# Kernel tuning notes

Hardware: AMD Instinct MI355X
Metric: run time of the kernel (lower is better)

Reference implementation:

```python
import jax, jax.numpy as jnp
import numpy as np

B, C, H, W = 4, 256, 48, 48
HEADS, DH = 8, 32
INNER = HEADS * DH
HID = 128  # max(16, INNER//2)
SCALE = DH ** -0.5
EPS = 1e-6


def setup_inputs() -> dict:
    key = jax.random.key(0)
    ks = jax.random.split(key, 32)
    s = 0.02
    inp = {
        'x': jax.random.normal(ks[0], (B, C, H, W), jnp.float32),
        'rgb_input': jax.random.uniform(ks[1], (B, 3, H, W), jnp.float32),
        'wq': jax.random.normal(ks[2], (INNER, C), jnp.float32) * s,
        'bq': jnp.zeros((INNER,), jnp.float32),
        'wk': jax.random.normal(ks[3], (INNER, C), jnp.float32) * s,
        'bk': jnp.zeros((INNER,), jnp.float32),
        'wv': jax.random.normal(ks[4], (INNER, C), jnp.float32) * s,
        'bv': jnp.zeros((INNER,), jnp.float32),
        'wproj': jax.random.normal(ks[5], (C, INNER), jnp.float32) * s,
        'bproj': jnp.zeros((C,), jnp.float32),
        'c1_w': jax.random.normal(ks[6], (HID, 1, 3, 3), jnp.float32) * s,
        'c1_b': jnp.zeros((HID,), jnp.float32),
        'c2_w': jax.random.normal(ks[7], (HID, HID, 3, 3), jnp.float32) * s,
        'c2_b': jnp.zeros((HID,), jnp.float32),
        'gq_w': jax.random.normal(ks[8], (INNER, HID), jnp.float32) * s,
        'gq_b': jnp.ones((INNER,), jnp.float32),
        'bqf_w': jax.random.normal(ks[9], (INNER, HID), jnp.float32) * s,
        'bqf_b': jnp.zeros((INNER,), jnp.float32),
        'gk_w': jax.random.normal(ks[10], (INNER, HID), jnp.float32) * s,
        'gk_b': jnp.ones((INNER,), jnp.float32),
        'bkf_w': jax.random.normal(ks[11], (INNER, HID), jnp.float32) * s,
        'bkf_b': jnp.zeros((INNER,), jnp.float32),
        'gv_w': jax.random.normal(ks[12], (INNER, HID), jnp.float32) * s,
        'gv_b': jnp.ones((INNER,), jnp.float32),
        'bvf_w': jax.random.normal(ks[13], (INNER, HID), jnp.float32) * s,
        'bvf_b': jnp.zeros((INNER,), jnp.float32),
        'alpha': jnp.float32(0.1),
    }
    return inp


def _conv3(x, w, b):
    y = jax.lax.conv_general_dilated(x, w, (1, 1), 'SAME',
                                     dimension_numbers=('NCHW', 'OIHW', 'NCHW'))
    return y + b[None, :, None, None]


def _rgb_to_luma(rgb):
    y = 0.299 * rgb[:, 0:1] + 0.587 * rgb[:, 1:2] + 0.114 * rgb[:, 2:3]
    y_min = jnp.min(y, axis=(2, 3), keepdims=True)
    y_max = jnp.max(y, axis=(2, 3), keepdims=True)
    return (y - y_min) / (y_max - y_min + EPS)


def reference(x, rgb_input, wq, bq, wk, bk, wv, bv, wproj, bproj,
              c1_w, c1_b, c2_w, c2_b,
              gq_w, gq_b, bqf_w, bqf_b, gk_w, gk_b, bkf_w, bkf_b,
              gv_w, gv_b, bvf_w, bvf_b, alpha):
    Bx, Cx, Hx, Wx = x.shape
    N = Hx * Wx
    luma = _rgb_to_luma(rgb_input)  # [B,1,H,W]

    # LumaCond trunk + FiLM params (1x1 convs then global spatial mean)
    h = jax.nn.relu(_conv3(luma, c1_w, c1_b))
    h = jax.nn.relu(_conv3(h, c2_w, c2_b))
    hm = h.mean(axis=(2, 3))  # [B,HID] (mean commutes with 1x1 conv)

    def film_params(gw, gb, bw, bb):
        g = hm @ gw.T + gb  # [B, INNER]
        bta = hm @ bw.T + bb
        return (g.reshape(Bx, HEADS, DH, 1), bta.reshape(Bx, HEADS, DH, 1))

    gq, fbq = film_params(gq_w, gq_b, bqf_w, bqf_b)
    gk, fbk = film_params(gk_w, gk_b, bkf_w, bkf_b)
    gv, fbv = film_params(gv_w, gv_b, bvf_w, bvf_b)

    def proj_film(w, b, g, bta):
        t = jnp.einsum('bchw,oc->bohw', x, w) + b[None, :, None, None]
        t = t.reshape(Bx, HEADS, DH, N)
        return g * t + bta  # [B,heads,dh,N]

    q = proj_film(wq, bq, gq, fbq)
    k = proj_film(wk, bk, gk, fbk)
    v = proj_film(wv, bv, gv, fbv)

    logits = jnp.einsum('bhdn,bhdm->bhnm', q, k) * SCALE  # [B,heads,N,N]

    # luma bias: avg-pooled inverse luma, mean-centered per image
    invL = 1.0 - luma
    invL = jax.lax.reduce_window(invL, 0.0, jax.lax.add,
                                 (1, 1, 3, 3), (1, 1, 1, 1), 'SAME') / 9.0
    invL = invL.reshape(Bx, N)
    invL = invL - invL.mean(axis=-1, keepdims=True)
    logits = logits + alpha * invL[:, None, None, :]

    attn = jax.nn.softmax(logits, axis=-1)
    out = jnp.einsum('bhnm,bhdm->bhdn', attn, v)  # [B,heads,dh,N]
    out = out.reshape(Bx, INNER, Hx, Wx)
    return jnp.einsum('bchw,oc->bohw', out, wproj) + bproj[None, :, None, None]
```

## Files before the change

kernel.cpp:

```cpp
#include <hip/hip_runtime.h>


#define NSP 2304
#define WID 48

typedef __attribute__((ext_vector_type(4))) float  fvec4;
typedef __attribute__((ext_vector_type(2))) unsigned int uvec2;
typedef __attribute__((ext_vector_type(4))) unsigned int uvec4;
typedef __attribute__((ext_vector_type(8))) short  short8;
typedef __attribute__((ext_vector_type(4))) float  f32x4;

__device__ inline unsigned short f2bf(float f){
  unsigned int u = __builtin_bit_cast(unsigned int, f);
  u += 0x7fffu + ((u >> 16) & 1u);
  return (unsigned short)(u >> 16);
}
__device__ inline unsigned pack2bf(float a, float b){
#if __has_builtin(__builtin_amdgcn_cvt_pk_bf16_f32)
  typedef __attribute__((ext_vector_type(2))) __bf16 bf16x2;
  bf16x2 r = __builtin_amdgcn_cvt_pk_bf16_f32(a, b);
  return __builtin_bit_cast(unsigned, r);
#else
  return (unsigned)f2bf(a) | ((unsigned)f2bf(b) << 16);
#endif
}

__global__ __launch_bounds__(256) void k_prep(const float* __restrict__ c2w,
    const float* __restrict__ wq, const float* __restrict__ wk, const float* __restrict__ wv_,
    const float* __restrict__ wproj, const float* __restrict__ x,
    const float* __restrict__ rgb, const float* __restrict__ alphaP,
    unsigned short* __restrict__ wtb, unsigned short* __restrict__ wqkvb,
    unsigned short* __restrict__ wprojb, unsigned short* __restrict__ xt,
    float* __restrict__ luma_n, float* __restrict__ bias_a,
    float* __restrict__ hm_sum, unsigned short* __restrict__ h1p){
  __shared__ __align__(16) float sm[5120];
  int bx = blockIdx.x, t = threadIdx.x;
  if (bx < 4){
    int b = bx;
    float* ly  = sm;
    float* ll  = sm + NSP;
    float* red = sm + 2*NSP;
    float* red2= sm + 2*NSP + 256;
    {
      const uvec4 z = {0u,0u,0u,0u};
      for (int j = t; j < 196*16; j += 256){
        int cell = j >> 4, q = j & 15;
        int r, c;
        if (cell < 50)      { r = 0;           c = cell; }
        else if (cell < 100){ r = 49;          c = cell - 50; }
        else if (cell < 148){ r = cell - 99;   c = 0; }
        else                { r = cell - 147;  c = 49; }
        *(uvec4*)(h1p + ((size_t)(b*2500 + r*50 + c))*128 + q*8) = z;
      }
    }
    const float* rp = rgb + b*3*NSP;
    float lmin = 1e30f, lmax = -1e30f;
    for (int i = t; i < NSP; i += 256){
      float y = 0.299f*rp[i] + 0.587f*rp[NSP+i] + 0.114f*rp[2*NSP+i];
      ly[i] = y; lmin = fminf(lmin, y); lmax = fmaxf(lmax, y);
    }
    red[t] = lmin; red2[t] = lmax;
    __syncthreads();
    for (int s = 128; s > 0; s >>= 1){
      if (t < s){ red[t] = fminf(red[t], red[t+s]); red2[t] = fmaxf(red2[t], red2[t+s]); }
      __syncthreads();
    }
    float mn = red[0], mx = red2[0];
    float inv = 1.0f / (mx - mn + 1e-6f);
    for (int i = t; i < NSP; i += 256){
      float v = (ly[i] - mn) * inv;
      ll[i] = v;
      luma_n[b*NSP + i] = v;
    }
    if (t < 128) hm_sum[b*128 + t] = 0.f;
    __syncthreads();
    float pr[9]; float psum = 0.f;
    #pragma unroll
    for (int ii = 0; ii < 9; ++ii){
      int n = t + 256*ii;
      int row = n / WID, col = n - row*WID;
      float s2 = 0.f;
      #pragma unroll
      for (int dy = -1; dy <= 1; ++dy)
        #pragma unroll
        for (int dx = -1; dx <= 1; ++dx){
          int r2 = row+dy, c2 = col+dx;
          if (r2 >= 0 && r2 < WID && c2 >= 0 && c2 < WID) s2 += 1.0f - ll[r2*WID + c2];
        }
      pr[ii] = s2 * (1.f/9.f);
      psum += pr[ii];
    }
    __syncthreads();
    red[t] = psum;
    __syncthreads();
    for (int s = 128; s > 0; s >>= 1){
      if (t < s) red[t] += red[t+s];
      __syncthreads();
    }
    float mean = red[0] * (1.f/(float)NSP);
    float alpha = alphaP[0] * 1.4426950408889634f;
    #pragma unroll
    for (int ii = 0; ii < 9; ++ii){
      int n = t + 256*ii;
      bias_a[b*NSP + n] = alpha * (pr[ii] - mean);
    }
  } else if (bx < 1604){
    int idx = (bx - 4)*256 + t;
    if (idx < 147456){
      int ic = idx & 127, rem = idx >> 7;
      int oc = rem & 127, tap = rem >> 7;
      wtb[idx] = f2bf(c2w[(oc*128 + ic)*9 + tap]);
    } else if (idx < 344064){
      int j = idx - 147456;
      int mat = j >> 16, oc_ = j & 65535;
      const float* src = (mat == 0) ? wq : (mat == 1) ? wk : wv_;
      wqkvb[j] = f2bf(src[oc_]);
    } else {
      int j = idx - 344064;
      wprojb[j] = f2bf(wproj[j]);
    }
  } else {
    int j = bx - 1604;
    int nt = j % 36, cc = (j / 36) & 3, b = j / 144;
    unsigned short* tb = (unsigned short*)sm;
    int cl0 = t >> 4;
    int nl0 = (t & 15) * 4;
    #pragma unroll
    for (int ps_ = 0; ps_ < 4; ++ps_){
      int cl = cl0 + ps_*16;
      fvec4 v = *(const fvec4*)(x + ((size_t)(b*256 + cc*64 + cl))*NSP + nt*64 + nl0);
      #pragma unroll
      for (int i = 0; i < 4; ++i) tb[(nl0+i)*72 + cl] = f2bf(v[i]);
    }
    __syncthreads();
    int nl = t >> 2, cg = (t & 3) * 16;
    uvec4 u0 = *(const uvec4*)&tb[nl*72 + cg];
    uvec4 u1 = *(const uvec4*)&tb[nl*72 + cg + 8];
    unsigned short* dst = xt + ((size_t)(b*NSP + nt*64 + nl))*256 + cc*64 + cg;
    *(uvec4*)dst = u0;
    *(uvec4*)(dst + 8) = u1;
  }
}

__global__ void k2_conv1(const float* __restrict__ luma_n, const float* __restrict__ c1w,
                         const float* __restrict__ c1b, unsigned short* __restrict__ h1p){
  int nt = blockIdx.x, ocg = blockIdx.y, b = blockIdx.z, t = threadIdx.x;
  __shared__ float wsm[32*9];
  __shared__ float bsm[32];
  for (int i = t; i < 288; i += 256) wsm[i] = c1w[ocg*288 + i];
  if (t < 32) bsm[t] = c1b[ocg*32 + t];
  __syncthreads();
  int n = nt*256 + t;
  int row = n / WID, col = n - row*WID;
  const float* lp = luma_n + b*NSP;
  float lv[9];
  int k = 0;
  #pragma unroll
  for (int dy = -1; dy <= 1; ++dy)
    #pragma unroll
    for (int dx = -1; dx <= 1; ++dx, ++k){
      int r2 = row+dy, c2 = col+dx;
      lv[k] = (r2 >= 0 && r2 < WID && c2 >= 0 && c2 < WID) ? lp[r2*WID + c2] : 0.f;
    }
  unsigned int packed[16];
  #pragma unroll
  for (int oc2 = 0; oc2 < 16; ++oc2){
    float a0 = bsm[oc2*2], a1 = bsm[oc2*2+1];
    #pragma unroll
    for (int q = 0; q < 9; ++q){
      a0 += wsm[(oc2*2)*9 + q] * lv[q];
      a1 += wsm[(oc2*2+1)*9 + q] * lv[q];
    }
    packed[oc2] = pack2bf(fmaxf(a0, 0.f), fmaxf(a1, 0.f));
  }
  unsigned short* dst = h1p + ((size_t)(b*2500 + (row+1)*50 + (col+1)))*128 + ocg*32;
  #pragma unroll
  for (int q4 = 0; q4 < 4; ++q4)
    *(uvec4*)(dst + q4*8) = *(uvec4*)&packed[q4*4];
}

__global__ __launch_bounds__(256) void k3_conv2(const unsigned short* __restrict__ h1p,
    const unsigned short* __restrict__ wtb, const float* __restrict__ c2b,
    float* __restrict__ hm_sum){
  int row = blockIdx.x, mh = blockIdx.y, b = blockIdx.z;
  int t = threadIdx.x, wv = t >> 6, lane = t & 63;
  int lq = lane >> 4, lc = lane & 15;
  int ocb = mh*64 + wv*16;
  const f32x4 z4 = {0.f, 0.f, 0.f, 0.f};
  f32x4 C[3] = {z4, z4, z4};
  const unsigned short* hbase = h1p + (size_t)b*2500*128;
  #pragma unroll
  for (int tap = 0; tap < 9; ++tap){
    int dy = tap/3 - 1, dx = tap%3 - 1;
    const unsigned short* wrow = wtb + (tap*128 + ocb + lc)*128 + lq*8;
    const unsigned short* hrow = hbase + ((row+dy+1)*50 + (dx+1) + lc)*128 + lq*8;
    #pragma unroll
    for (int kc = 0; kc < 4; ++kc){
      short8 aW = *(const short8*)(wrow + kc*32);
      #pragma unroll
      for (int ntp = 0; ntp < 3; ++ntp){
        short8 bH = *(const short8*)(hrow + ntp*16*128 + kc*32);
        C[ntp] = __builtin_amdgcn_mfma_f32_16x16x32_bf16(aW, bH, C[ntp], 0, 0, 0);
      }
    }
  }
  float s[4];
  #pragma unroll
  for (int r = 0; r < 4; ++r){
    float bias = c2b[ocb + lq*4 + r];
    float v = 0.f;
    #pragma unroll
    for (int ntp = 0; ntp < 3; ++ntp) v += fmaxf(C[ntp][r] + bias, 0.f);
    v += __shfl_xor(v, 1, 64);
    v += __shfl_xor(v, 2, 64);
    v += __shfl_xor(v, 4, 64);
    v += __shfl_xor(v, 8, 64);
    s[r] = v;
  }
  if (lc == 0){
    #pragma unroll
    for (int r = 0; r < 4; ++r)
      atomicAdd(&hm_sum[b*128 + ocb + lq*4 + r], s[r]);
  }
}

__global__ void k4_film(const float* __restrict__ hm_sum,
  const float* w0, const float* b0, const float* w1, const float* b1,
  const float* w2, const float* b2, const float* w3, const float* b3,
  const float* w4, const float* b4, const float* w5, const float* b5,
  float* __restrict__ film){
  __shared__ float hs[128];
  int bb = blockIdx.x & 3, m6 = blockIdx.x >> 2, t = threadIdx.x;
  if (t < 128) hs[t] = hm_sum[bb*128 + t] * (1.f/(float)NSP);
  __syncthreads();
  const float* wm[6] = {w0,w1,w2,w3,w4,w5};
  const float* bm[6] = {b0,b1,b2,b3,b4,b5};
  const float* w = wm[m6];
  int o = t;
  float a = bm[m6][o];
  for (int h2 = 0; h2 < 128; ++h2) a += hs[h2] * w[o*128 + h2];
  film[blockIdx.x*256 + t] = a;
}

__global__ __launch_bounds__(256) void k5_qkv(const unsigned short* __restrict__ xt,
    const unsigned short* __restrict__ wqkvb,
    const float* __restrict__ bq, const float* __restrict__ bk, const float* __restrict__ bv,
    const float* __restrict__ film,
    unsigned short* __restrict__ q_t, unsigned short* __restrict__ k_t,
    unsigned short* __restrict__ v_b){
  int nt = blockIdx.x, ot = blockIdx.y, b = blockIdx.z;
  int t = threadIdx.x, wv = t >> 6, lane = t & 63;
  int lq = lane >> 4, lc = lane & 15;
  int p = ot >> 1;
  int omb = (ot & 1)*128 + wv*32;
  const f32x4 z4 = {0.f, 0.f, 0.f, 0.f};
  f32x4 acc[2][4];
  #pragma unroll
  for (int oh = 0; oh < 2; ++oh)
    #pragma unroll
    for (int nq = 0; nq < 4; ++nq) acc[oh][nq] = z4;

  const unsigned short* wbp = wqkvb + p*65536 + (omb + lc)*256 + lq*8;
  const unsigned short* xbp = xt + ((size_t)(b*NSP + nt*64 + lc))*256 + lq*8;

  short8 aW0[2], aW1[2], bX0[4], bX1[4];
  auto loadW = [&](short8 (&W)[2], int kc){
    #pragma unroll
    for (int oh = 0; oh < 2; ++oh) W[oh] = *(const short8*)(wbp + oh*16*256 + kc*32);
  };
  auto loadX = [&](short8 (&X)[4], int kc){
    #pragma unroll
    for (int nq = 0; nq < 4; ++nq) X[nq] = *(const short8*)(xbp + (size_t)nq*16*256 + kc*32);
  };
  auto mm = [&](short8 (&W)[2], short8 (&X)[4]){
    #pragma unroll
    for (int oh = 0; oh < 2; ++oh)
      #pragma unroll
      for (int nq = 0; nq < 4; ++nq)
        acc[oh][nq] = __builtin_amdgcn_mfma_f32_16x16x32_bf16(W[oh], X[nq], acc[oh][nq], 0, 0, 0);
  };
  loadW(aW0, 0); loadX(bX0, 0);
  for (int kc2 = 0; kc2 < 4; ++kc2){
    loadW(aW1, kc2*2+1); loadX(bX1, kc2*2+1);
    mm(aW0, bX0);
    int kn = (kc2*2+2) & 7;
    loadW(aW0, kn); loadX(bX0, kn);
    mm(aW1, bX1);
  }

  const float* bvec = (p == 0) ? bq : (p == 1) ? bk : bv;
  int hq = omb >> 5;
  unsigned short* qk = (p == 0) ? q_t : k_t;
  #pragma unroll
  for (int oh = 0; oh < 2; ++oh){
    fvec4 g4 = *(const fvec4*)(film + (2*p*4 + b)*256 + omb + oh*16 + lq*4);
    fvec4 t4 = *(const fvec4*)(film + ((2*p+1)*4 + b)*256 + omb + oh*16 + lq*4);
    fvec4 z4b = *(const fvec4*)(bvec + omb + oh*16 + lq*4);
    #pragma unroll
    for (int nq = 0; nq < 4; ++nq){
      int n = nt*64 + nq*16 + lc;
      float v0 = g4[0]*(acc[oh][nq][0] + z4b[0]) + t4[0];
      float v1 = g4[1]*(acc[oh][nq][1] + z4b[1]) + t4[1];
      float v2 = g4[2]*(acc[oh][nq][2] + z4b[2]) + t4[2];
      float v3 = g4[3]*(acc[oh][nq][3] + z4b[3]) + t4[3];
      if (p == 0){
        const float sc = 0.17677669529663687f * 1.4426950408889634f;
        v0 *= sc; v1 *= sc; v2 *= sc; v3 *= sc;
      }
      if (p < 2){
        uvec2 u;
        u.x = pack2bf(v0, v1);
        u.y = pack2bf(v2, v3);
        *(uvec2*)(qk + ((size_t)((b*8 + hq)*NSP + n))*32 + oh*16 + lq*4) = u;
      } else {
        int om = omb + oh*16 + lq*4;
        v_b[((size_t)(b*256 + om + 0))*NSP + n] = f2bf(v0);
        v_b[((size_t)(b*256 + om + 1))*NSP + n] = f2bf(v1);
        v_b[((size_t)(b*256 + om + 2))*NSP + n] = f2bf(v2);
        v_b[((size_t)(b*256 + om + 3))*NSP + n] = f2bf(v3);
      }
    }
  }
}

__global__ __launch_bounds__(256, 4) void k6_attn(const unsigned short* __restrict__ q_t,
    const unsigned short* __restrict__ k_t, const unsigned short* __restrict__ v_b,
    const float* __restrict__ bias_a,
    unsigned short* __restrict__ o0, unsigned short* __restrict__ o1,
    float* __restrict__ l0, float* __restrict__ l1){
  int bx = blockIdx.x, h = blockIdx.y, b = blockIdx.z;
  int qblk = bx >> 1, s = bx & 1;
  unsigned short* op = s ? o1 : o0;
  float* lp = s ? l1 : l0;
  int t = threadIdx.x, wv = t >> 6, lane = t & 63;
  int lq = lane >> 4, lc = lane & 15;
  int bh = b*8 + h;
  int nb0 = qblk*128 + wv*32;
  const f32x4 z4 = {0.f, 0.f, 0.f, 0.f};
  int ms = s*1152;

  __shared__ unsigned short Kb[2][64*32];
  __shared__ unsigned short Vb[2][32*64];
  __shared__ float ps[4][1024];

  const unsigned short* kg = k_t + ((size_t)bh*NSP + ms + (t>>2))*32 + (t&3)*8;
  const unsigned short* vg = v_b + ((size_t)(b*256 + h*32 + (t>>3)))*NSP + ms + (t&7)*8;
  int krow = t >> 2;
  unsigned short* kw = &Kb[0][krow*32 + (((t&3) ^ ((krow>>1)&3))*8)];
  int vrow = t >> 3;
  unsigned short* vw = &Vb[0][vrow*64 + (((t&7) ^ (vrow&7))*8)];

  int kcol = (lq ^ ((lc>>1)&3))*8;
  int sxm = ((lc&7)<<2) | (((lc>>3)&1)<<1);
  int wbase = lc*32;

  const float* brow = bias_a + b*NSP + ms;
  fvec4 c0r[4];
  #pragma unroll
  for (int g = 0; g < 4; ++g) c0r[g] = *(const fvec4*)(brow + g*16 + lq*4);

  short8 aQ[2];
  #pragma unroll
  for (int qf = 0; qf < 2; ++qf)
    aQ[qf] = *(const short8*)(q_t + ((size_t)(bh*NSP + nb0 + qf*16 + lc))*32 + lq*8);

  uvec4 gKr = *(const uvec4*)kg;
  uvec4 gVr = *(const uvec4*)vg;

  const uvec4 onesu = {0x3F803F80u, 0x3F803F80u, 0x3F803F80u, 0x3F803F80u};
  const short8 aOnes = __builtin_bit_cast(short8, onesu);

  f32x4 O[2][2]; f32x4 Ol[2];
  #pragma unroll
  for (int qf = 0; qf < 2; ++qf){
    Ol[qf] = z4; O[qf][0] = z4; O[qf][1] = z4;
  }
  float* myps = ps[wv];

  for (int it = 0; it < 18; ++it){
    int buf = it & 1;
    *(uvec4*)(kw + buf*2048) = gKr;
    *(uvec4*)(vw + buf*2048) = gVr;
    __syncthreads();
    if (it < 17){
      gKr = *(const uvec4*)(kg + (it+1)*2048);
      gVr = *(const uvec4*)(vg + (it+1)*64);
    }
    const unsigned short* kb = Kb[buf];
    const unsigned short* vb = Vb[buf];
    short8 aK[4], aV[2][2];
    #pragma unroll
    for (int g = 0; g < 4; ++g)
      aK[g] = *(const short8*)(kb + (g*16 + lc)*32 + kcol);
    #pragma unroll
    for (int dhg = 0; dhg < 2; ++dhg)
      #pragma unroll
      for (int mh = 0; mh < 2; ++mh)
        aV[dhg][mh] = *(const short8*)(vb + (dhg*16 + lc)*64 + (((mh*4 + lq) ^ (lc&7))*8));
    #pragma unroll
    for (int qf = 0; qf < 2; ++qf){
      #pragma unroll
      for (int g = 0; g < 4; ++g){
        f32x4 S = __builtin_amdgcn_mfma_f32_16x16x32_bf16(aK[g], aQ[qf], c0r[g], 0, 0, 0);
        uvec2 w2;
        w2.x = pack2bf(__builtin_amdgcn_exp2f(S[0]), __builtin_amdgcn_exp2f(S[1]));
        w2.y = pack2bf(__builtin_amdgcn_exp2f(S[2]), __builtin_amdgcn_exp2f(S[3]));
        *(uvec2*)&myps[qf*512 + wbase + ((g*8 + lq*2) ^ sxm)] = w2;
      }
    }
    if (it < 17){
      #pragma unroll
      for (int g = 0; g < 4; ++g)
        c0r[g] = *(const fvec4*)(brow + (it+1)*64 + g*16 + lq*4);
    }
    __builtin_amdgcn_s_setprio(1);
    #pragma unroll
    for (int qf = 0; qf < 2; ++qf){
      #pragma unroll
      for (int mh = 0; mh < 2; ++mh){
        int d0 = (mh*16 + lq*4) ^ sxm;
        uvec2 lo = *(const uvec2*)&myps[qf*512 + wbase + d0];
        uvec2 hi = *(const uvec2*)&myps[qf*512 + wbase + (d0 ^ 2)];
        uvec4 up; up.x = lo.x; up.y = lo.y; up.z = hi.x; up.w = hi.y;
        short8 bP = __builtin_bit_cast(short8, up);
        Ol[qf] = __builtin_amdgcn_mfma_f32_16x16x32_bf16(aOnes, bP, Ol[qf], 0, 0, 0);
        #pragma unroll
        for (int dhg = 0; dhg < 2; ++dhg)
          O[qf][dhg] = __builtin_amdgcn_mfma_f32_16x16x32_bf16(aV[dhg][mh], bP, O[qf][dhg], 0, 0, 0);
      }
    }
    __builtin_amdgcn_s_setprio(0);
  }
  #pragma unroll
  for (int qf = 0; qf < 2; ++qf){
    int nidx = nb0 + qf*16 + lc;
    if (lq == 0) lp[b*NSP + nidx] = Ol[qf][0];
    #pragma unroll
    for (int dh = 0; dh < 2; ++dh){
      uvec2 u;
      u.x = pack2bf(O[qf][dh][0], O[qf][dh][1]);
      u.y = pack2bf(O[qf][dh][2], O[qf][dh][3]);
      *(uvec2*)(op + ((size_t)(b*NSP + nidx))*256 + h*32 + dh*16 + lq*4) = u;
    }
  }
}

__global__ __launch_bounds__(256) void k7_proj(const unsigned short* __restrict__ a0,
    const unsigned short* __restrict__ a1, const float* __restrict__ l0p,
    const float* __restrict__ l1p, const unsigned short* __restrict__ wprojb,
    const float* __restrict__ bproj, float* __restrict__ out){
  int nt = blockIdx.x, ct = blockIdx.y, b = blockIdx.z;
  int t = threadIdx.x, wv = t >> 6, lane = t & 63;
  int lq = lane >> 4, lc = lane & 15;
  __shared__ float rls[32];
  if (t < 32) rls[t] = 1.0f / (l0p[b*NSP + nt*32 + t] + l1p[b*NSP + nt*32 + t]);
  __syncthreads();
  int cb = ct*128 + wv*32;
  const f32x4 z4 = {0.f, 0.f, 0.f, 0.f};
  f32x4 acc[2][2];
  #pragma unroll
  for (int ch = 0; ch < 2; ++ch)
    #pragma unroll
    for (int nq = 0; nq < 2; ++nq) acc[ch][nq] = z4;

  const unsigned short* wpp = wprojb + (cb + lc)*256 + lq*8;
  const unsigned short* a0p = a0 + ((size_t)(b*NSP + nt*32 + lc))*256 + lq*8;
  const unsigned short* a1p = a1 + ((size_t)(b*NSP + nt*32 + lc))*256 + lq*8;

  short8 W0[2], W1[2], p00[2], p01[2], p10[2], p11[2];
  auto loadS = [&](short8 (&W)[2], short8 (&B0)[2], short8 (&B1)[2], int kc){
    #pragma unroll
    for (int ch = 0; ch < 2; ++ch) W[ch] = *(const short8*)(wpp + ch*16*256 + kc*32);
    #pragma unroll
    for (int nq = 0; nq < 2; ++nq){
      B0[nq] = *(const short8*)(a0p + (size_t)nq*16*256 + kc*32);
      B1[nq] = *(const short8*)(a1p + (size_t)nq*16*256 + kc*32);
    }
  };
  auto mmS = [&](short8 (&W)[2], short8 (&B0)[2], short8 (&B1)[2]){
    #pragma unroll
    for (int ch = 0; ch < 2; ++ch)
      #pragma unroll
      for (int nq = 0; nq < 2; ++nq){
        acc[ch][nq] = __builtin_amdgcn_mfma_f32_16x16x32_bf16(W[ch], B0[nq], acc[ch][nq], 0, 0, 0);
        acc[ch][nq] = __builtin_amdgcn_mfma_f32_16x16x32_bf16(W[ch], B1[nq], acc[ch][nq], 0, 0, 0);
      }
  };
  loadS(W0, p00, p10, 0);
  for (int kc2 = 0; kc2 < 4; ++kc2){
    loadS(W1, p01, p11, kc2*2+1);
    mmS(W0, p00, p10);
    int kn = (kc2*2+2) & 7;
    loadS(W0, p00, p10, kn);
    mmS(W1, p01, p11);
  }

  #pragma unroll
  for (int ch = 0; ch < 2; ++ch){
    #pragma unroll
    for (int nq = 0; nq < 2; ++nq){
      int n = nt*32 + nq*16 + lc;
      float rl = rls[nq*16 + lc];
      #pragma unroll
      for (int r = 0; r < 4; ++r){
        int c = cb + ch*16 + lq*4 + r;
        out[((size_t)(b*256 + c))*NSP + n] = acc[ch][nq][r]*rl + bproj[c];
      }
    }
  }
}

extern "C" void kernel_launch(void* const* d_in, const int* in_sizes, int n_in,
                              void* d_out, int out_size, void* d_ws, size_t ws_size,
                              hipStream_t stream) {
  const float* x     = (const float*)d_in[0];
  const float* rgb   = (const float*)d_in[1];
  const float* wq    = (const float*)d_in[2];
  const float* bq    = (const float*)d_in[3];
  const float* wk    = (const float*)d_in[4];
  const float* bk    = (const float*)d_in[5];
  const float* wv    = (const float*)d_in[6];
  const float* bv    = (const float*)d_in[7];
  const float* wproj = (const float*)d_in[8];
  const float* bproj = (const float*)d_in[9];
  const float* c1w   = (const float*)d_in[10];
  const float* c1b   = (const float*)d_in[11];
  const float* c2w   = (const float*)d_in[12];
  const float* c2b   = (const float*)d_in[13];
  const float* gq_w  = (const float*)d_in[14];
  const float* gq_b  = (const float*)d_in[15];
  const float* bqf_w = (const float*)d_in[16];
  const float* bqf_b = (const float*)d_in[17];
  const float* gk_w  = (const float*)d_in[18];
  const float* gk_b  = (const float*)d_in[19];
  const float* bkf_w = (const float*)d_in[20];
  const float* bkf_b = (const float*)d_in[21];
  const float* gv_w  = (const float*)d_in[22];
  const float* gv_b  = (const float*)d_in[23];
  const float* bvf_w = (const float*)d_in[24];
  const float* bvf_b = (const float*)d_in[25];
  const float* alphaP= (const float*)d_in[26];

  char* w = (char*)d_ws;
  float* luma_n = (float*)w;            w += 4*NSP*4;
  float* bias_a = (float*)w;            w += 4*NSP*4;
  float* hm_sum = (float*)w;            w += 512*4;
  float* film   = (float*)w;            w += 6*4*256*4;
  unsigned short* h1p = (unsigned short*)w; w += 4*2500*128*2;
  unsigned short* wtb = (unsigned short*)w; w += 9*128*128*2;
  unsigned short* wqkvb = (unsigned short*)w; w += 3*256*256*2;
  unsigned short* wprojb = (unsigned short*)w; w += 256*256*2;
  unsigned short* xt  = (unsigned short*)w; w += (size_t)4*NSP*256*2;
  unsigned short* q_t = (unsigned short*)w; w += (size_t)4*8*NSP*32*2;
  unsigned short* k_t = (unsigned short*)w; w += (size_t)4*8*NSP*32*2;
  unsigned short* v_b = (unsigned short*)w; w += (size_t)4*256*NSP*2;
  unsigned short* o_part0 = (unsigned short*)w; w += (size_t)4*NSP*256*2;
  unsigned short* o_part1 = (unsigned short*)w; w += (size_t)4*NSP*256*2;
  float* l_part0 = (float*)w;           w += 4*NSP*4;
  float* l_part1 = (float*)w;           w += 4*NSP*4;

  k_prep  <<<2180, 256, 0, stream>>>(c2w, wq, wk, wv, wproj, x, rgb, alphaP,
                                     wtb, wqkvb, wprojb, xt,
                                     luma_n, bias_a, hm_sum, h1p);
  k2_conv1<<<dim3(9,4,4), 256, 0, stream>>>(luma_n, c1w, c1b, h1p);
  k3_conv2<<<dim3(48,2,4), 256, 0, stream>>>(h1p, wtb, c2b, hm_sum);
  k4_film <<<24, 256, 0, stream>>>(hm_sum, gq_w, gq_b, bqf_w, bqf_b,
                                   gk_w, gk_b, bkf_w, bkf_b,
                                   gv_w, gv_b, bvf_w, bvf_b, film);
  k5_qkv  <<<dim3(36,6,4), 256, 0, stream>>>(xt, wqkvb, bq, bk, bv, film,
                                             q_t, k_t, v_b);
  k6_attn <<<dim3(36,8,4), 256, 0, stream>>>(q_t, k_t, v_b, bias_a,
                                             o_part0, o_part1, l_part0, l_part1);
  k7_proj <<<dim3(72,2,4), 256, 0, stream>>>(o_part0, o_part1, l_part0, l_part1,
                                             wprojb, bproj, (float*)d_out);
}
```

Baseline: 261.0 us.

## Split attention key range three ways and halve per-wave P scratch

The attention kernel now splits the key dimension into three chunks of 768 instead of two of 1152, launching 54×8×4 blocks so the grid fills the GPU better. The projection kernel sums three partial outputs and denominators, and the third partial reuses the xt buffer, which is no longer needed after QKV. The P scratch per wave is halved by handling each query fragment's exp/store and PV MFMAs in turn, which cuts LDS use and may raise occupancy. The cost is an extra partial buffer to read and write and more MFMAs in the projection.

Result: no change. 261.1 us (+0.0%).

```diff
diff --git a/kernel.cpp b/kernel.cpp
--- a/kernel.cpp
+++ b/kernel.cpp
@@ -327,21 +327,22 @@
     const unsigned short* __restrict__ k_t, const unsigned short* __restrict__ v_b,
     const float* __restrict__ bias_a,
     unsigned short* __restrict__ o0, unsigned short* __restrict__ o1,
-    float* __restrict__ l0, float* __restrict__ l1){
+    unsigned short* __restrict__ o2,
+    float* __restrict__ l0, float* __restrict__ l1, float* __restrict__ l2){
   int bx = blockIdx.x, h = blockIdx.y, b = blockIdx.z;
-  int qblk = bx >> 1, s = bx & 1;
-  unsigned short* op = s ? o1 : o0;
-  float* lp = s ? l1 : l0;
+  int qblk = bx / 3, s = bx - qblk*3;
+  unsigned short* op = (s == 0) ? o0 : (s == 1) ? o1 : o2;
+  float* lp = (s == 0) ? l0 : (s == 1) ? l1 : l2;
   int t = threadIdx.x, wv = t >> 6, lane = t & 63;
   int lq = lane >> 4, lc = lane & 15;
   int bh = b*8 + h;
   int nb0 = qblk*128 + wv*32;
   const f32x4 z4 = {0.f, 0.f, 0.f, 0.f};
-  int ms = s*1152;
+  int ms = s*768;
 
   __shared__ unsigned short Kb[2][64*32];
   __shared__ unsigned short Vb[2][32*64];
-  __shared__ float ps[4][1024];
+  __shared__ float ps[4][512];
 
   const unsigned short* kg = k_t + ((size_t)bh*NSP + ms + (t>>2))*32 + (t&3)*8;
   const unsigned short* vg = v_b + ((size_t)(b*256 + h*32 + (t>>3)))*NSP + ms + (t&7)*8;
@@ -377,12 +378,12 @@
   }
   float* myps = ps[wv];
 
-  for (int it = 0; it < 18; ++it){
+  for (int it = 0; it < 12; ++it){
     int buf = it & 1;
     *(uvec4*)(kw + buf*2048) = gKr;
     *(uvec4*)(vw + buf*2048) = gVr;
     __syncthreads();
-    if (it < 17){
+    if (it < 11){
       gKr = *(const uvec4*)(kg + (it+1)*2048);
       gVr = *(const uvec4*)(vg + (it+1)*64);
     }
@@ -405,22 +406,19 @@
         uvec2 w2;
         w2.x = pack2bf(__builtin_amdgcn_exp2f(S[0]), __builtin_amdgcn_exp2f(S[1]));
         w2.y = pack2bf(__builtin_amdgcn_exp2f(S[2]), __builtin_amdgcn_exp2f(S[3]));
-        *(uvec2*)&myps[qf*512 + wbase + ((g*8 + lq*2) ^ sxm)] = w2;
-      }
-    }
-    if (it < 17){
-      #pragma unroll
-      for (int g = 0; g < 4; ++g)
-        c0r[g] = *(const fvec4*)(brow + (it+1)*64 + g*16 + lq*4);
-    }
-    __builtin_amdgcn_s_setprio(1);
-    #pragma unroll
-    for (int qf = 0; qf < 2; ++qf){
+        *(uvec2*)&myps[wbase + ((g*8 + lq*2) ^ sxm)] = w2;
+      }
+      if (qf == 1 && it < 11){
+        #pragma unroll
+        for (int g = 0; g < 4; ++g)
+          c0r[g] = *(const fvec4*)(brow + (it+1)*64 + g*16 + lq*4);
+      }
+      __builtin_amdgcn_s_setprio(1);
       #pragma unroll
       for (int mh = 0; mh < 2; ++mh){
         int d0 = (mh*16 + lq*4) ^ sxm;
-        uvec2 lo = *(const uvec2*)&myps[qf*512 + wbase + d0];
-        uvec2 hi = *(const uvec2*)&myps[qf*512 + wbase + (d0 ^ 2)];
+        uvec2 lo = *(const uvec2*)&myps[wbase + d0];
+        uvec2 hi = *(const uvec2*)&myps[wbase + (d0 ^ 2)];
         uvec4 up; up.x = lo.x; up.y = lo.y; up.z = hi.x; up.w = hi.y;
         short8 bP = __builtin_bit_cast(short8, up);
         Ol[qf] = __builtin_amdgcn_mfma_f32_16x16x32_bf16(aOnes, bP, Ol[qf], 0, 0, 0);
@@ -428,8 +426,8 @@
         for (int dhg = 0; dhg < 2; ++dhg)
           O[qf][dhg] = __builtin_amdgcn_mfma_f32_16x16x32_bf16(aV[dhg][mh], bP, O[qf][dhg], 0, 0, 0);
       }
-    }
-    __builtin_amdgcn_s_setprio(0);
+      __builtin_amdgcn_s_setprio(0);
+    }
   }
   #pragma unroll
   for (int qf = 0; qf < 2; ++qf){
@@ -446,14 +444,16 @@
 }
 
 __global__ __launch_bounds__(256) void k7_proj(const unsigned short* __restrict__ a0,
-    const unsigned short* __restrict__ a1, const float* __restrict__ l0p,
-    const float* __restrict__ l1p, const unsigned short* __restrict__ wprojb,
+    const unsigned short* __restrict__ a1, const unsigned short* __restrict__ a2,
+    const float* __restrict__ l0p, const float* __restrict__ l1p,
+    const float* __restrict__ l2p, const unsigned short* __restrict__ wprojb,
     const float* __restrict__ bproj, float* __restrict__ out){
   int nt = blockIdx.x, ct = blockIdx.y, b = blockIdx.z;
   int t = threadIdx.x, wv = t >> 6, lane = t & 63;
   int lq = lane >> 4, lc = lane & 15;
   __shared__ float rls[32];
-  if (t < 32) rls[t] = 1.0f / (l0p[b*NSP + nt*32 + t] + l1p[b*NSP + nt*32 + t]);
+  if (t < 32) rls[t] = 1.0f / (l0p[b*NSP + nt*32 + t] + l1p[b*NSP + nt*32 + t]
+                               + l2p[b*NSP + nt*32 + t]);
   __syncthreads();
   int cb = ct*128 + wv*32;
   const f32x4 z4 = {0.f, 0.f, 0.f, 0.f};
@@ -466,33 +466,35 @@
   const unsigned short* wpp = wprojb + (cb + lc)*256 + lq*8;
   const unsigned short* a0p = a0 + ((size_t)(b*NSP + nt*32 + lc))*256 + lq*8;
   const unsigned short* a1p = a1 + ((size_t)(b*NSP + nt*32 + lc))*256 + lq*8;
-
-  short8 W0[2], W1[2], p00[2], p01[2], p10[2], p11[2];
-  auto loadS = [&](short8 (&W)[2], short8 (&B0)[2], short8 (&B1)[2], int kc){
+  const unsigned short* a2p = a2 + ((size_t)(b*NSP + nt*32 + lc))*256 + lq*8;
+
+  short8 W0[2], W1[2], B0[3][2], B1[3][2];
+  auto loadS = [&](short8 (&W)[2], short8 (&B)[3][2], int kc){
     #pragma unroll
     for (int ch = 0; ch < 2; ++ch) W[ch] = *(const short8*)(wpp + ch*16*256 + kc*32);
     #pragma unroll
     for (int nq = 0; nq < 2; ++nq){
-      B0[nq] = *(const short8*)(a0p + (size_t)nq*16*256 + kc*32);
-      B1[nq] = *(const short8*)(a1p + (size_t)nq*16*256 + kc*32);
+      B[0][nq] = *(const short8*)(a0p + (size_t)nq*16*256 + kc*32);
+      B[1][nq] = *(const short8*)(a1p + (size_t)nq*16*256 + kc*32);
+      B[2][nq] = *(const short8*)(a2p + (size_t)nq*16*256 + kc*32);
     }
   };
-  auto mmS = [&](short8 (&W)[2], short8 (&B0)[2], short8 (&B1)[2]){
-    #pragma unroll
-    for (int ch = 0; ch < 2; ++ch)
-      #pragma unroll
-      for (int nq = 0; nq < 2; ++nq){
-        acc[ch][nq] = __builtin_amdgcn_mfma_f32_16x16x32_bf16(W[ch], B0[nq], acc[ch][nq], 0, 0, 0);
-        acc[ch][nq] = __builtin_amdgcn_mfma_f32_16x16x32_bf16(W[ch], B1[nq], acc[ch][nq], 0, 0, 0);
-      }
+  auto mmS = [&](short8 (&W)[2], short8 (&B)[3][2]){
+    #pragma unroll
+    for (int src = 0; src < 3; ++src)
+      #pragma unroll
+      for (int ch = 0; ch < 2; ++ch)
+        #pragma unroll
+        for (int nq = 0; nq < 2; ++nq)
+          acc[ch][nq] = __builtin_amdgcn_mfma_f32_16x16x32_bf16(W[ch], B[src][nq], acc[ch][nq], 0, 0, 0);
   };
-  loadS(W0, p00, p10, 0);
+  loadS(W0, B0, 0);
   for (int kc2 = 0; kc2 < 4; ++kc2){
-    loadS(W1, p01, p11, kc2*2+1);
-    mmS(W0, p00, p10);
+    loadS(W1, B1, kc2*2+1);
+    mmS(W0, B0);
     int kn = (kc2*2+2) & 7;
-    loadS(W0, p00, p10, kn);
-    mmS(W1, p01, p11);
+    loadS(W0, B0, kn);
+    mmS(W1, B1);
   }
 
   #pragma unroll
@@ -558,6 +560,8 @@
   unsigned short* o_part1 = (unsigned short*)w; w += (size_t)4*NSP*256*2;
   float* l_part0 = (float*)w;           w += 4*NSP*4;
   float* l_part1 = (float*)w;           w += 4*NSP*4;
+  float* l_part2 = (float*)w;           w += 4*NSP*4;
+  unsigned short* o_part2 = xt;
 
   k_prep  <<<2180, 256, 0, stream>>>(c2w, wq, wk, wv, wproj, x, rgb, alphaP,
                                      wtb, wqkvb, wprojb, xt,
@@ -569,8 +573,10 @@
                                    gv_w, gv_b, bvf_w, bvf_b, film);
   k5_qkv  <<<dim3(36,6,4), 256, 0, stream>>>(xt, wqkvb, bq, bk, bv, film,
                                              q_t, k_t, v_b);
-  k6_attn <<<dim3(36,8,4), 256, 0, stream>>>(q_t, k_t, v_b, bias_a,
-                                             o_part0, o_part1, l_part0, l_part1);
-  k7_proj <<<dim3(72,2,4), 256, 0, stream>>>(o_part0, o_part1, l_part0, l_part1,
+  k6_attn <<<dim3(54,8,4), 256, 0, stream>>>(q_t, k_t, v_b, bias_a,
+                                             o_part0, o_part1, o_part2,
+                                             l_part0, l_part1, l_part2);
+  k7_proj <<<dim3(72,2,4), 256, 0, stream>>>(o_part0, o_part1, o_part2,
+                                             l_part0, l_part1, l_part2,
                                              wprojb, bproj, (float*)d_out);
 }
```

## Fuse conv1, conv2 and FiLM kernels into one launch with grid barriers

Applied to the files above, without the earlier changes.

Merges the three small FiLM-path kernels (conv1, conv2 reduction, FiLM linear) into a single 384-block kernel. The stages are separated by software grid barriers built on global atomic counters, which k_prep resets. The goal is to remove two kernel launch gaps and their tail drain. In exchange it relies on all 384 blocks being co-resident to avoid deadlock, and it adds spin-wait cost on the barriers.

Measured after the change: 389.3 us. +49.2%, slower.

```diff
diff --git a/kernel.cpp b/kernel.cpp
--- a/kernel.cpp
+++ b/kernel.cpp
@@ -32,11 +32,13 @@
     unsigned short* __restrict__ wtb, unsigned short* __restrict__ wqkvb,
     unsigned short* __restrict__ wprojb, unsigned short* __restrict__ xt,
     float* __restrict__ luma_n, float* __restrict__ bias_a,
-    float* __restrict__ hm_sum, unsigned short* __restrict__ h1p){
+    float* __restrict__ hm_sum, unsigned short* __restrict__ h1p,
+    int* __restrict__ syncc){
   __shared__ __align__(16) float sm[5120];
   int bx = blockIdx.x, t = threadIdx.x;
   if (bx < 4){
     int b = bx;
+    if (bx == 0 && t < 4) syncc[t] = 0;
     float* ly  = sm;
     float* ll  = sm + NSP;
     float* red = sm + 2*NSP;
@@ -142,104 +144,125 @@
   }
 }
 
-__global__ void k2_conv1(const float* __restrict__ luma_n, const float* __restrict__ c1w,
-                         const float* __restrict__ c1b, unsigned short* __restrict__ h1p){
-  int nt = blockIdx.x, ocg = blockIdx.y, b = blockIdx.z, t = threadIdx.x;
-  __shared__ float wsm[32*9];
-  __shared__ float bsm[32];
-  for (int i = t; i < 288; i += 256) wsm[i] = c1w[ocg*288 + i];
-  if (t < 32) bsm[t] = c1b[ocg*32 + t];
+__global__ __launch_bounds__(256) void k_film(const float* __restrict__ luma_n,
+    const float* __restrict__ c1w, const float* __restrict__ c1b,
+    unsigned short* __restrict__ h1p,
+    const unsigned short* __restrict__ wtb, const float* __restrict__ c2b,
+    float* __restrict__ hm_sum,
+    const float* w0, const float* b0, const float* w1, const float* b1,
+    const float* w2, const float* b2, const float* w3, const float* b3,
+    const float* w4, const float* b4, const float* w5, const float* b5,
+    float* __restrict__ film, int* __restrict__ syncc){
+  int g = blockIdx.x, t = threadIdx.x;
+  __shared__ __align__(16) float sm2[320];
+
+  if (g < 144){
+    int nt = g % 9, ocg = (g/9) & 3, b = g / 36;
+    float* wsm = sm2;
+    float* bsm = sm2 + 288;
+    for (int i = t; i < 288; i += 256) wsm[i] = c1w[ocg*288 + i];
+    if (t < 32) bsm[t] = c1b[ocg*32 + t];
+    __syncthreads();
+    int n = nt*256 + t;
+    int row = n / WID, col = n - row*WID;
+    const float* lp = luma_n + b*NSP;
+    float lv[9];
+    int k = 0;
+    #pragma unroll
+    for (int dy = -1; dy <= 1; ++dy)
+      #pragma unroll
+      for (int dx = -1; dx <= 1; ++dx, ++k){
+        int r2 = row+dy, c2 = col+dx;
+        lv[k] = (r2 >= 0 && r2 < WID && c2 >= 0 && c2 < WID) ? lp[r2*WID + c2] : 0.f;
+      }
+    unsigned int packed[16];
+    #pragma unroll
+    for (int oc2 = 0; oc2 < 16; ++oc2){
+      float a0 = bsm[oc2*2], a1 = bsm[oc2*2+1];
+      #pragma unroll
+      for (int q = 0; q < 9; ++q){
+        a0 += wsm[(oc2*2)*9 + q] * lv[q];
+        a1 += wsm[(oc2*2+1)*9 + q] * lv[q];
+      }
+      packed[oc2] = pack2bf(fmaxf(a0, 0.f), fmaxf(a1, 0.f));
+    }
+    unsigned short* dst = h1p + ((size_t)(b*2500 + (row+1)*50 + (col+1)))*128 + ocg*32;
+    #pragma unroll
+    for (int q4 = 0; q4 < 4; ++q4)
+      *(uvec4*)(dst + q4*8) = *(uvec4*)&packed[q4*4];
+  }
+
   __syncthreads();
-  int n = nt*256 + t;
-  int row = n / WID, col = n - row*WID;
-  const float* lp = luma_n + b*NSP;
-  float lv[9];
-  int k = 0;
-  #pragma unroll
-  for (int dy = -1; dy <= 1; ++dy)
-    #pragma unroll
-    for (int dx = -1; dx <= 1; ++dx, ++k){
-      int r2 = row+dy, c2 = col+dx;
-      lv[k] = (r2 >= 0 && r2 < WID && c2 >= 0 && c2 < WID) ? lp[r2*WID + c2] : 0.f;
-    }
-  unsigned int packed[16];
-  #pragma unroll
-  for (int oc2 = 0; oc2 < 16; ++oc2){
-    float a0 = bsm[oc2*2], a1 = bsm[oc2*2+1];
-    #pragma unroll
-    for (int q = 0; q < 9; ++q){
-      a0 += wsm[(oc2*2)*9 + q] * lv[q];
-      a1 += wsm[(oc2*2+1)*9 + q] * lv[q];
-    }
-    packed[oc2] = pack2bf(fmaxf(a0, 0.f), fmaxf(a1, 0.f));
-  }
-  unsigned short* dst = h1p + ((size_t)(b*2500 + (row+1)*50 + (col+1)))*128 + ocg*32;
-  #pragma unroll
-  for (int q4 = 0; q4 < 4; ++q4)
-    *(uvec4*)(dst + q4*8) = *(uvec4*)&packed[q4*4];
-}
-
-__global__ __launch_bounds__(256) void k3_conv2(const unsigned short* __restrict__ h1p,
-    const unsigned short* __restrict__ wtb, const float* __restrict__ c2b,
-    float* __restrict__ hm_sum){
-  int row = blockIdx.x, mh = blockIdx.y, b = blockIdx.z;
-  int t = threadIdx.x, wv = t >> 6, lane = t & 63;
-  int lq = lane >> 4, lc = lane & 15;
-  int ocb = mh*64 + wv*16;
-  const f32x4 z4 = {0.f, 0.f, 0.f, 0.f};
-  f32x4 C[3] = {z4, z4, z4};
-  const unsigned short* hbase = h1p + (size_t)b*2500*128;
-  #pragma unroll
-  for (int tap = 0; tap < 9; ++tap){
-    int dy = tap/3 - 1, dx = tap%3 - 1;
-    const unsigned short* wrow = wtb + (tap*128 + ocb + lc)*128 + lq*8;
-    const unsigned short* hrow = hbase + ((row+dy+1)*50 + (dx+1) + lc)*128 + lq*8;
-    #pragma unroll
-    for (int kc = 0; kc < 4; ++kc){
-      short8 aW = *(const short8*)(wrow + kc*32);
-      #pragma unroll
-      for (int ntp = 0; ntp < 3; ++ntp){
-        short8 bH = *(const short8*)(hrow + ntp*16*128 + kc*32);
-        C[ntp] = __builtin_amdgcn_mfma_f32_16x16x32_bf16(aW, bH, C[ntp], 0, 0, 0);
-      }
-    }
-  }
-  float s[4];
-  #pragma unroll
-  for (int r = 0; r < 4; ++r){
-    float bias = c2b[ocb + lq*4 + r];
-    float v = 0.f;
-    #pragma unroll
-    for (int ntp = 0; ntp < 3; ++ntp) v += fmaxf(C[ntp][r] + bias, 0.f);
-    v += __shfl_xor(v, 1, 64);
-    v += __shfl_xor(v, 2, 64);
-    v += __shfl_xor(v, 4, 64);
-    v += __shfl_xor(v, 8, 64);
-    s[r] = v;
-  }
-  if (lc == 0){
-    #pragma unroll
-    for (int r = 0; r < 4; ++r)
-      atomicAdd(&hm_sum[b*128 + ocb + lq*4 + r], s[r]);
-  }
-}
-
-__global__ void k4_film(const float* __restrict__ hm_sum,
-  const float* w0, const float* b0, const float* w1, const float* b1,
-  const float* w2, const float* b2, const float* w3, const float* b3,
-  const float* w4, const float* b4, const float* w5, const float* b5,
-  float* __restrict__ film){
-  __shared__ float hs[128];
-  int bb = blockIdx.x & 3, m6 = blockIdx.x >> 2, t = threadIdx.x;
-  if (t < 128) hs[t] = hm_sum[bb*128 + t] * (1.f/(float)NSP);
+  if (t == 0){
+    __threadfence();
+    __hip_atomic_fetch_add(&syncc[0], 1, __ATOMIC_ACQ_REL, __HIP_MEMORY_SCOPE_AGENT);
+    while (__hip_atomic_load(&syncc[0], __ATOMIC_ACQUIRE, __HIP_MEMORY_SCOPE_AGENT) < 384){}
+  }
   __syncthreads();
-  const float* wm[6] = {w0,w1,w2,w3,w4,w5};
-  const float* bm[6] = {b0,b1,b2,b3,b4,b5};
-  const float* w = wm[m6];
-  int o = t;
-  float a = bm[m6][o];
-  for (int h2 = 0; h2 < 128; ++h2) a += hs[h2] * w[o*128 + h2];
-  film[blockIdx.x*256 + t] = a;
+
+  {
+    int row = g % 48, mh = (g/48) & 1, b = g / 96;
+    int wv = t >> 6, lane = t & 63;
+    int lq = lane >> 4, lc = lane & 15;
+    int ocb = mh*64 + wv*16;
+    const f32x4 z4 = {0.f, 0.f, 0.f, 0.f};
+    f32x4 C[3] = {z4, z4, z4};
+    const unsigned short* hbase = h1p + (size_t)b*2500*128;
+    #pragma unroll
+    for (int tap = 0; tap < 9; ++tap){
+      int dy = tap/3 - 1, dx = tap%3 - 1;
+      const unsigned short* wrow = wtb + (tap*128 + ocb + lc)*128 + lq*8;
+      const unsigned short* hrow = hbase + ((row+dy+1)*50 + (dx+1) + lc)*128 + lq*8;
+      #pragma unroll
+      for (int kc = 0; kc < 4; ++kc){
+        short8 aW = *(const short8*)(wrow + kc*32);
+        #pragma unroll
+        for (int ntp = 0; ntp < 3; ++ntp){
+          short8 bH = *(const short8*)(hrow + ntp*16*128 + kc*32);
+          C[ntp] = __builtin_amdgcn_mfma_f32_16x16x32_bf16(aW, bH, C[ntp], 0, 0, 0);
+        }
+      }
+    }
+    float s[4];
+    #pragma unroll
+    for (int r = 0; r < 4; ++r){
+      float bias = c2b[ocb + lq*4 + r];
+      float v = 0.f;
+      #pragma unroll
+      for (int ntp = 0; ntp < 3; ++ntp) v += fmaxf(C[ntp][r] + bias, 0.f);
+      v += __shfl_xor(v, 1, 64);
+      v += __shfl_xor(v, 2, 64);
+      v += __shfl_xor(v, 4, 64);
+      v += __shfl_xor(v, 8, 64);
+      s[r] = v;
+    }
+    if (lc == 0){
+      #pragma unroll
+      for (int r = 0; r < 4; ++r)
+        atomicAdd(&hm_sum[b*128 + ocb + lq*4 + r], s[r]);
+    }
+  }
+
+  if (t == 0){
+    __threadfence();
+    __hip_atomic_fetch_add(&syncc[1], 1, __ATOMIC_ACQ_REL, __HIP_MEMORY_SCOPE_AGENT);
+    while (__hip_atomic_load(&syncc[1], __ATOMIC_ACQUIRE, __HIP_MEMORY_SCOPE_AGENT) < 384){}
+  }
+  __syncthreads();
+
+  if (g < 24){
+    float* hs = sm2;
+    int bb = g & 3, m6 = g >> 2;
+    if (t < 128) hs[t] = hm_sum[bb*128 + t] * (1.f/(float)NSP);
+    __syncthreads();
+    const float* wm[6] = {w0,w1,w2,w3,w4,w5};
+    const float* bm[6] = {b0,b1,b2,b3,b4,b5};
+    const float* w = wm[m6];
+    int o = t;
+    float a = bm[m6][o];
+    for (int h2 = 0; h2 < 128; ++h2) a += hs[h2] * w[o*128 + h2];
+    film[g*256 + t] = a;
+  }
 }
 
 __global__ __launch_bounds__(256) void k5_qkv(const unsigned short* __restrict__ xt,
@@ -546,6 +569,7 @@
   float* bias_a = (float*)w;            w += 4*NSP*4;
   float* hm_sum = (float*)w;            w += 512*4;
   float* film   = (float*)w;            w += 6*4*256*4;
+  int*   syncc  = (int*)w;              w += 16;
   unsigned short* h1p = (unsigned short*)w; w += 4*2500*128*2;
   unsigned short* wtb = (unsigned short*)w; w += 9*128*128*2;
   unsigned short* wqkvb = (unsigned short*)w; w += 3*256*256*2;
@@ -561,12 +585,12 @@
 
   k_prep  <<<2180, 256, 0, stream>>>(c2w, wq, wk, wv, wproj, x, rgb, alphaP,
                                      wtb, wqkvb, wprojb, xt,
-                                     luma_n, bias_a, hm_sum, h1p);
-  k2_conv1<<<dim3(9,4,4), 256, 0, stream>>>(luma_n, c1w, c1b, h1p);
-  k3_conv2<<<dim3(48,2,4), 256, 0, stream>>>(h1p, wtb, c2b, hm_sum);
-  k4_film <<<24, 256, 0, stream>>>(hm_sum, gq_w, gq_b, bqf_w, bqf_b,
-                                   gk_w, gk_b, bkf_w, bkf_b,
-                                   gv_w, gv_b, bvf_w, bvf_b, film);
+                                     luma_n, bias_a, hm_sum, h1p, syncc);
+  k_film  <<<384, 256, 0, stream>>>(luma_n, c1w, c1b, h1p, wtb, c2b, hm_sum,
+                                    gq_w, gq_b, bqf_w, bqf_b,
+                                    gk_w, gk_b, bkf_w, bkf_b,
+                                    gv_w, gv_b, bvf_w, bvf_b,
+                                    film, syncc);
   k5_qkv  <<<dim3(36,6,4), 256, 0, stream>>>(xt, wqkvb, bq, bk, bv, film,
                                              q_t, k_t, v_b);
   k6_attn <<<dim3(36,8,4), 256, 0, stream>>>(q_t, k_t, v_b, bias_a,
```
